# Kernel optimization log

Measured on AMD Instinct MI355X. Metric: run time of the kernel, lower is better.

Reference implementation:

```python
import jax, jax.numpy as jnp
import numpy as np

DIM = 768
NUM_HEADS = 12
HEAD_DIM = 64  # attn_head_dim override
ALL_HEAD_DIM = NUM_HEADS * HEAD_DIM  # 768
SCALE = HEAD_DIM ** -0.5


def setup_inputs() -> dict:
    key = jax.random.key(0)
    ks = jax.random.split(key, 6)
    B, N = 8, 1024
    x = jax.random.normal(ks[0], (B, N, DIM), dtype=jnp.float32)
    w_qkv = jax.random.normal(ks[1], (3 * ALL_HEAD_DIM, DIM), dtype=jnp.float32) * (DIM ** -0.5)
    q_bias = jnp.zeros((ALL_HEAD_DIM,), dtype=jnp.float32)
    v_bias = jnp.zeros((ALL_HEAD_DIM,), dtype=jnp.float32)
    w_proj = jax.random.normal(ks[2], (DIM, ALL_HEAD_DIM), dtype=jnp.float32) * (ALL_HEAD_DIM ** -0.5)
    b_proj = jnp.zeros((DIM,), dtype=jnp.float32)
    return {"x": x, "w_qkv": w_qkv, "q_bias": q_bias, "v_bias": v_bias,
            "w_proj": w_proj, "b_proj": b_proj}


def reference(x, w_qkv, q_bias, v_bias, w_proj, b_proj):
    B, N, C = x.shape
    # qkv bias: [q_bias, zeros (k has no bias), v_bias]
    qkv_bias = jnp.concatenate([q_bias, jnp.zeros_like(v_bias), v_bias])
    qkv = x @ w_qkv.T + qkv_bias                      # [B, N, 3*ALL_HEAD_DIM]
    qkv = qkv.reshape(B, N, 3, NUM_HEADS, HEAD_DIM).transpose(2, 0, 3, 1, 4)
    q, k, v = qkv[0], qkv[1], qkv[2]                  # each [B, H, N, D]
    attn = jnp.einsum('bhqd,bhkd->bhqk', q * SCALE, k)
    attn = jax.nn.softmax(attn, axis=-1)
    out = jnp.einsum('bhqk,bhkd->bhqd', attn, v)      # [B, H, N, D]
    out = out.transpose(0, 2, 1, 3).reshape(B, N, ALL_HEAD_DIM)
    out = out @ w_proj.T + b_proj                     # [B, N, C]
    return out
```

## Files before the change

kernel.cpp:

```cpp
#include <hip/hip_runtime.h>
#include <hip/hip_bf16.h>

typedef unsigned short u16;
typedef unsigned int u32;
typedef __attribute__((ext_vector_type(4))) float f32x4;
typedef __attribute__((ext_vector_type(16))) float f32x16;
typedef __attribute__((ext_vector_type(8))) short bf16x8;

__device__ inline u16 f2bf(float f) {
    union { float f; u32 u; } v; v.f = f;
    u32 r = v.u + 0x7fff + ((v.u >> 16) & 1);
    return (u16)(r >> 16);
}

__device__ inline f32x4 mfma16(bf16x8 a, bf16x8 b, f32x4 c) {
    return __builtin_amdgcn_mfma_f32_16x16x32_bf16(a, b, c, 0, 0, 0);
}
__device__ inline f32x16 mfma32(bf16x8 a, bf16x8 b, f32x16 c) {
    return __builtin_amdgcn_mfma_f32_32x32x16_bf16(a, b, c, 0, 0, 0);
}
__device__ inline u32 cvtpk(float lo, float hi) {
    u32 r;
    asm("v_cvt_pk_bf16_f32 %0, %1, %2" : "=v"(r) : "v"(lo), "v"(hi));
    return r;
}
__device__ inline float exp2v(float x) {
    float r;
    asm("v_exp_f32 %0, %1" : "=v"(r) : "v"(x));
    return r;
}

__device__ inline void gload_lds16(const void* g, const void* l) {
    __builtin_amdgcn_global_load_lds(
        (const __attribute__((address_space(1))) void*)g,
        (__attribute__((address_space(3))) void*)l, 16, 0, 0);
}

#define QSCALE 0.18033688f

__global__ void cvt_all(const float* __restrict__ x,
                        const float* __restrict__ wq,
                        const float* __restrict__ wp,
                        u16* __restrict__ xb, u16* __restrict__ wqb,
                        u16* __restrict__ wpb) {
    int i = blockIdx.x * 256 + threadIdx.x;
    const float* src; u16* dst; int off;
    if (i < 786432)       { src = x;  dst = xb;  off = i; }
    else if (i < 1007616) { src = wq; dst = wqb; off = i - 786432; }
    else                  { src = wp; dst = wpb; off = i - 1007616; }
    const float4* p = (const float4*)src;
    float4 a = p[2 * off], b = p[2 * off + 1];
    bf16x8 v;
    v[0] = (short)f2bf(a.x); v[1] = (short)f2bf(a.y);
    v[2] = (short)f2bf(a.z); v[3] = (short)f2bf(a.w);
    v[4] = (short)f2bf(b.x); v[5] = (short)f2bf(b.y);
    v[6] = (short)f2bf(b.z); v[7] = (short)f2bf(b.w);
    ((bf16x8*)dst)[off] = v;
}

template <int EPI>
__global__ __launch_bounds__(256) void gemm_bt2(
    const u16* __restrict__ A, const u16* __restrict__ B,
    int nbn,
    u16* __restrict__ qw, u16* __restrict__ kw, u16* __restrict__ vw,
    const float* __restrict__ qb, const float* __restrict__ vb,
    float* __restrict__ outp, const float* __restrict__ bproj)
{
    __shared__ __align__(16) u16 smem[16384];
    const int K = 768;
    const int NT = 24;
    const int tid = threadIdx.x;
    const int lane = tid & 63, wv = tid >> 6;
    const int nwg = gridDim.x;
    const int wg = (blockIdx.x & 7) * (nwg >> 3) + (blockIdx.x >> 3);
    const int bm = wg / nbn, bn = wg % nbn;
    const int row0 = bm << 7, col0 = bn << 7;

    const int srow = tid >> 2;
    const int sch = (tid & 3) ^ ((srow >> 1) & 3);
    const u16* gA = A + (size_t)(row0 + srow) * K + sch * 8;
    const u16* gB = B + (size_t)(col0 + srow) * K + sch * 8;
    const int ldst = wv * 512;

    auto stageTile = [&](int bufi, int t) {
        u16* base = &smem[bufi * 8192];
        const int k0 = t << 5;
        gload_lds16(gA + k0,                   base + ldst);
        gload_lds16(gA + (size_t)64 * K + k0,  base + 2048 + ldst);
        gload_lds16(gB + k0,                   base + 4096 + ldst);
        gload_lds16(gB + (size_t)64 * K + k0,  base + 4096 + 2048 + ldst);
    };

    const int wr = (wv >> 1) << 6;
    const int wc = (wv & 1) << 6;
    const int arl = lane & 15, ahi = lane >> 4;
    bf16x8 fa[4], fb[4];
    auto loadFrags = [&](int bufi) {
        const u16* bA = &smem[bufi * 8192];
        const u16* bB = &smem[bufi * 8192 + 4096];
#pragma unroll
        for (int fi = 0; fi < 4; ++fi) {
            const int rl = wr + fi * 16 + arl;
            fa[fi] = *(const bf16x8*)(bA + rl * 32 + ((ahi ^ ((rl >> 1) & 3)) << 3));
        }
#pragma unroll
        for (int fj = 0; fj < 4; ++fj) {
            const int cl = wc + fj * 16 + arl;
            fb[fj] = *(const bf16x8*)(bB + cl * 32 + ((ahi ^ ((cl >> 1) & 3)) << 3));
        }
    };

    f32x4 acc[4][4];
#pragma unroll
    for (int i = 0; i < 4; i++)
#pragma unroll
        for (int j = 0; j < 4; j++) acc[i][j] = (f32x4){0.f, 0.f, 0.f, 0.f};

    auto mfmaTile = [&]() {
        __builtin_amdgcn_s_setprio(1);
#pragma unroll
        for (int i = 0; i < 4; i++)
#pragma unroll
            for (int j = 0; j < 4; j++)
                acc[i][j] = mfma16(fa[i], fb[j], acc[i][j]);
        __builtin_amdgcn_s_setprio(0);
    };

    stageTile(0, 0); stageTile(1, 1);

#pragma unroll 1
    for (int t = 0; t < NT - 1; ++t) {
        asm volatile("s_waitcnt vmcnt(4)" ::: "memory");
        __builtin_amdgcn_s_barrier();
        loadFrags(t & 1);
        asm volatile("s_waitcnt lgkmcnt(0)" ::: "memory");
        __builtin_amdgcn_sched_barrier(0);
        __builtin_amdgcn_s_barrier();
        if (t < NT - 2) stageTile(t & 1, t + 2);
        __builtin_amdgcn_sched_barrier(0);
        mfmaTile();
    }
    asm volatile("s_waitcnt vmcnt(0)" ::: "memory");
    __builtin_amdgcn_s_barrier();
    loadFrags((NT - 1) & 1);
    asm volatile("s_waitcnt lgkmcnt(0)" ::: "memory");
    __builtin_amdgcn_sched_barrier(0);
    mfmaTile();
    __syncthreads();

    if (EPI == 0) {
        const int part = col0 / 768;
        const int colr0 = col0 - part * 768;
        const int h0 = colr0 >> 6;
        const int bb = row0 >> 10;
        const int n0 = row0 & 1023;

        if (part < 2) {
#pragma unroll
            for (int nj = 0; nj < 4; ++nj) {
                const int col = wc + nj * 16 + arl;
                const float bias = (part == 0) ? qb[colr0 + col] : 0.f;
                const float sc = (part == 0) ? QSCALE : 1.f;
#pragma unroll
                for (int mi = 0; mi < 4; ++mi) {
#pragma unroll
                    for (int j = 0; j < 4; ++j) {
                        const int row = wr + mi * 16 + (ahi << 2) + j;
                        smem[row * 128 + ((((col >> 3) ^ (row & 7)) << 3) | (col & 7))] =
                            f2bf((acc[mi][nj][j] + bias) * sc);
                    }
                }
            }
        } else {
#pragma unroll
            for (int nj = 0; nj < 4; ++nj) {
                const int col = wc + nj * 16 + arl;
                const float bias = vb[colr0 + col];
#pragma unroll
                for (int mi = 0; mi < 4; ++mi) {
                    const int row = wr + mi * 16 + (ahi << 2);
                    ushort4 pk;
                    pk.x = f2bf(acc[mi][nj][0] + bias);
                    pk.y = f2bf(acc[mi][nj][1] + bias);
                    pk.z = f2bf(acc[mi][nj][2] + bias);
                    pk.w = f2bf(acc[mi][nj][3] + bias);
                    *(ushort4*)&smem[col * 128 +
                        ((((row >> 3) ^ (col & 7)) << 3) | (row & 7))] = pk;
                }
            }
        }
        __syncthreads();

        if (part == 0) {
#pragma unroll
            for (int p = 0; p < 8; ++p) {
                const int c = p * 256 + tid;
                const int h = c >> 10, ri = (c >> 3) & 127, j = c & 7;
                bf16x8 v = *(const bf16x8*)&smem[ri * 128 + ((((h << 3) + j) ^ (ri & 7)) << 3)];
                *(bf16x8*)&qw[((size_t)(((bb * 12 + h0 + h) << 10) + n0 + ri)) * 64 + j * 8] = v;
            }
        } else if (part == 1) {
#pragma unroll
            for (int p = 0; p < 8; ++p) {
                const int c = p * 256 + tid;
                const int h = c >> 10, t2 = (c >> 8) & 3, j = (c >> 5) & 7, r = c & 31;
                const int ri = t2 * 32 + r;
                bf16x8 v = *(const bf16x8*)&smem[ri * 128 + ((((h << 3) + j) ^ (ri & 7)) << 3)];
                *(bf16x8*)&kw[((size_t)(bb * 12 + h0 + h) << 16) +
                              (((n0 >> 5) + t2) << 11) + (j << 8) + (r << 3)] = v;
            }
        } else {
#pragma unroll
            for (int p = 0; p < 8; ++p) {
                const int c = p * 256 + tid;
                const int h = c >> 10, w = c & 1023;
                const int t2 = w >> 8, f = (w >> 6) & 3, ln = w & 63;
                const int d = ((f >> 1) << 5) + (ln & 31);
                const int rb_ = t2 * 32 + ((f & 1) << 4) + ((ln >> 5) << 3);
                const int ct = h * 64 + d;
                bf16x8 v = *(const bf16x8*)&smem[ct * 128 + (((rb_ >> 3) ^ (ct & 7)) << 3)];
                *(bf16x8*)&vw[((size_t)(bb * 12 + h0 + h) << 16) +
                              (((n0 >> 5) + t2) << 11) + (f << 9) + (ln << 3)] = v;
            }
        }
    } else {
        const int N = nbn << 7;
#pragma unroll
        for (int nj = 0; nj < 4; ++nj) {
            const int col = col0 + wc + nj * 16 + arl;
            const float bias = bproj[col];
#pragma unroll
            for (int mi = 0; mi < 4; ++mi) {
#pragma unroll
                for (int j = 0; j < 4; ++j) {
                    const int row = row0 + wr + mi * 16 + (ahi << 2) + j;
                    outp[(size_t)row * N + col] = acc[mi][nj][j] + bias;
                }
            }
        }
    }
}

__global__ __launch_bounds__(256, 3) void attn_fwd(
    const u16* __restrict__ Q, const u16* __restrict__ KF,
    const u16* __restrict__ VF, u16* __restrict__ O)
{
    __shared__ __align__(16) u16 tlds[4][32 * 68];
    const int tid = threadIdx.x, lane = tid & 63, wv = tid >> 6;
    const int l31 = lane & 31, hi = lane >> 5;
    const int bh = blockIdx.x % 96;
    const int qbk = blockIdx.x / 96;
    const int q0 = qbk * 128 + wv * 32;
    const size_t base = (size_t)bh << 16;
    const u16* Qp = Q + base;
    const u16* Kp = KF + base;
    const u16* Vp = VF + base;

    bf16x8 qf0, qf1, qf2, qf3;
    {
        const u16* qrow = &Qp[(q0 + l31) * 64 + hi * 8];
        qf0 = *(const bf16x8*)(qrow);
        qf1 = *(const bf16x8*)(qrow + 16);
        qf2 = *(const bf16x8*)(qrow + 32);
        qf3 = *(const bf16x8*)(qrow + 48);
    }

    f32x16 ot0, ot1;
#pragma unroll
    for (int i = 0; i < 16; ++i) { ot0[i] = 0.f; ot1[i] = 0.f; }
    float m = -1e30f, l = 0.f;

    auto loadK = [&](int t2048, bf16x8& f0, bf16x8& f1, bf16x8& f2, bf16x8& f3) {
        const u16* kr = &Kp[t2048 + hi * 256 + l31 * 8];
        f0 = *(const bf16x8*)(kr);
        f1 = *(const bf16x8*)(kr + 512);
        f2 = *(const bf16x8*)(kr + 1024);
        f3 = *(const bf16x8*)(kr + 1536);
    };

    auto body = [&](int t2048, bf16x8 k0, bf16x8 k1, bf16x8 k2, bf16x8 k3) {
        f32x16 s;
#pragma unroll
        for (int i = 0; i < 16; ++i) s[i] = 0.f;
        __builtin_amdgcn_s_setprio(1);
        s = mfma32(k0, qf0, s);
        s = mfma32(k1, qf1, s);
        s = mfma32(k2, qf2, s);
        s = mfma32(k3, qf3, s);
        __builtin_amdgcn_s_setprio(0);
        const u16* vrow = &Vp[t2048 + lane * 8];
        bf16x8 vf00 = *(const bf16x8*)(vrow);
        bf16x8 vf01 = *(const bf16x8*)(vrow + 512);
        bf16x8 vf10 = *(const bf16x8*)(vrow + 1024);
        bf16x8 vf11 = *(const bf16x8*)(vrow + 1536);
        float t0 = fmaxf(fmaxf(s[0], s[1]), fmaxf(s[2], s[3]));
        float t1 = fmaxf(fmaxf(s[4], s[5]), fmaxf(s[6], s[7]));
        float t2 = fmaxf(fmaxf(s[8], s[9]), fmaxf(s[10], s[11]));
        float t3 = fmaxf(fmaxf(s[12], s[13]), fmaxf(s[14], s[15]));
        float tmax = fmaxf(fmaxf(t0, t1), fmaxf(t2, t3));
        tmax = fmaxf(tmax, __shfl_xor(tmax, 32));
        if (!__all(tmax - m <= 8.f)) {
            const float nm = fmaxf(m, tmax);
            const float cr = exp2v(m - nm);
#pragma unroll
            for (int i = 0; i < 16; ++i) { ot0[i] *= cr; ot1[i] *= cr; }
            l *= cr; m = nm;
        }
#pragma unroll
        for (int i = 0; i < 16; ++i) { float p = exp2v(s[i] - m); s[i] = p; l += p; }
        u32 w0 = cvtpk(s[0],  s[1]),  w1 = cvtpk(s[2],  s[3]);
        u32 w2 = cvtpk(s[4],  s[5]),  w3 = cvtpk(s[6],  s[7]);
        u32 w4 = cvtpk(s[8],  s[9]),  w5 = cvtpk(s[10], s[11]);
        u32 w6 = cvtpk(s[12], s[13]), w7 = cvtpk(s[14], s[15]);
        asm("v_permlane32_swap_b32 %0, %1" : "+v"(w0), "+v"(w2));
        asm("v_permlane32_swap_b32 %0, %1" : "+v"(w1), "+v"(w3));
        asm("v_permlane32_swap_b32 %0, %1" : "+v"(w4), "+v"(w6));
        asm("v_permlane32_swap_b32 %0, %1" : "+v"(w5), "+v"(w7));
        union { u32 u[4]; bf16x8 v; } pb0, pb1;
        pb0.u[0] = w0; pb0.u[1] = w1; pb0.u[2] = w2; pb0.u[3] = w3;
        pb1.u[0] = w4; pb1.u[1] = w5; pb1.u[2] = w6; pb1.u[3] = w7;
        __builtin_amdgcn_s_setprio(1);
        ot0 = mfma32(vf00, pb0.v, ot0);
        ot0 = mfma32(vf01, pb1.v, ot0);
        ot1 = mfma32(vf10, pb0.v, ot1);
        ot1 = mfma32(vf11, pb1.v, ot1);
        __builtin_amdgcn_s_setprio(0);
    };

    bf16x8 ka0, ka1, ka2, ka3, kb0, kb1, kb2, kb3;
    loadK(0, ka0, ka1, ka2, ka3);
    for (int kt = 0; kt < 32; kt += 2) {
        loadK((kt + 1) << 11, kb0, kb1, kb2, kb3);
        body(kt << 11, ka0, ka1, ka2, ka3);
        if (kt + 2 < 32) loadK((kt + 2) << 11, ka0, ka1, ka2, ka3);
        body((kt + 1) << 11, kb0, kb1, kb2, kb3);
    }

    const float lt = l + __shfl_xor(l, 32);
    const float inv = 1.f / lt;
    u16* tw = &tlds[wv][0];
    u32* tw32 = (u32*)tw;
#pragma unroll
    for (int i = 0; i < 8; ++i) {
        const int dl = 2 * (i & 1) + 8 * (i >> 1) + 4 * hi;
        tw32[(l31 * 68 + dl) >> 1]      = cvtpk(ot0[2 * i] * inv, ot0[2 * i + 1] * inv);
        tw32[(l31 * 68 + dl + 32) >> 1] = cvtpk(ot1[2 * i] * inv, ot1[2 * i + 1] * inv);
    }
    __syncthreads();
    const int b = bh / 12, h = bh - b * 12;
    const size_t obase = ((size_t)(b << 10) + q0) * 768 + h * 64 + (lane & 7) * 8;
#pragma unroll
    for (int it = 0; it < 4; ++it) {
        const int r = it * 8 + (lane >> 3);
        bf16x8 v = *(const bf16x8*)&tw[r * 68 + (lane & 7) * 8];
        *(bf16x8*)&O[obase + (size_t)r * 768] = v;
    }
}

extern "C" void kernel_launch(void* const* d_in, const int* in_sizes, int n_in,
                              void* d_out, int out_size, void* d_ws, size_t ws_size,
                              hipStream_t stream) {
    const float* x      = (const float*)d_in[0];
    const float* w_qkv  = (const float*)d_in[1];
    const float* q_bias = (const float*)d_in[2];
    const float* v_bias = (const float*)d_in[3];
    const float* w_proj = (const float*)d_in[4];
    const float* b_proj = (const float*)d_in[5];
    float* out = (float*)d_out;

    char* ws = (char*)d_ws;
    u16* xb     = (u16*)(ws);
    u16* wqkvb  = (u16*)(ws + 12582912);
    u16* wprojb = (u16*)(ws + 16121856);
    u16* qw     = (u16*)(ws + 17301504);
    u16* kw     = (u16*)(ws + 29884416);
    u16* vt     = (u16*)(ws + 42467328);
    u16* ob     = (u16*)(ws + 55050240);

    cvt_all<<<4224, 256, 0, stream>>>(x, w_qkv, w_proj, xb, wqkvb, wprojb);

    gemm_bt2<0><<<(8192 / 128) * (2304 / 128), 256, 0, stream>>>(
        xb, wqkvb, 2304 / 128, qw, kw, vt, q_bias, v_bias, nullptr, nullptr);

    attn_fwd<<<96 * 8, 256, 0, stream>>>(qw, kw, vt, ob);

    gemm_bt2<1><<<(8192 / 128) * (768 / 128), 256, 0, stream>>>(
        ob, wprojb, 768 / 128, nullptr, nullptr, nullptr, nullptr, nullptr, out, b_proj);
}
```

Baseline: 110.2 us.

## Pre-swizzle weights into fragment layout and load B directly from global

The conversion kernel now writes the bf16 weight matrices in a tiled fragment-ready layout (128-col by 32-k tiles). The GEMM then loads B fragments straight from global/L2 into registers instead of staging them through LDS. Only A remains double-buffered in shared memory. This cuts LDS traffic and halves the async loads per stage, but the B loads are now exposed global latency inside the loop rather than prefetched two tiles ahead.

```diff
diff --git a/kernel.cpp b/kernel.cpp
--- a/kernel.cpp
+++ b/kernel.cpp
@@ -44,10 +44,10 @@
                         u16* __restrict__ xb, u16* __restrict__ wqb,
                         u16* __restrict__ wpb) {
     int i = blockIdx.x * 256 + threadIdx.x;
-    const float* src; u16* dst; int off;
-    if (i < 786432)       { src = x;  dst = xb;  off = i; }
-    else if (i < 1007616) { src = wq; dst = wqb; off = i - 786432; }
-    else                  { src = wp; dst = wpb; off = i - 1007616; }
+    const float* src; u16* dst; int off; bool frag;
+    if (i < 786432)       { src = x;  dst = xb;  off = i;           frag = false; }
+    else if (i < 1007616) { src = wq; dst = wqb; off = i - 786432;  frag = true;  }
+    else                  { src = wp; dst = wpb; off = i - 1007616; frag = true;  }
     const float4* p = (const float4*)src;
     float4 a = p[2 * off], b = p[2 * off + 1];
     bf16x8 v;
@@ -55,12 +55,18 @@
     v[2] = (short)f2bf(a.z); v[3] = (short)f2bf(a.w);
     v[4] = (short)f2bf(b.x); v[5] = (short)f2bf(b.y);
     v[6] = (short)f2bf(b.z); v[7] = (short)f2bf(b.w);
-    ((bf16x8*)dst)[off] = v;
+    if (!frag) {
+        ((bf16x8*)dst)[off] = v;
+    } else {
+        const int n = off / 96, k8 = off - n * 96;
+        const int addr = (((n >> 7) * 24 + (k8 >> 2)) << 12) + ((n & 127) << 5) + ((k8 & 3) << 3);
+        *(bf16x8*)&dst[addr] = v;
+    }
 }
 
 template <int EPI>
-__global__ __launch_bounds__(256) void gemm_bt2(
-    const u16* __restrict__ A, const u16* __restrict__ B,
+__global__ __launch_bounds__(256) void gemm_bL2(
+    const u16* __restrict__ A, const u16* __restrict__ Bf,
     int nbn,
     u16* __restrict__ qw, u16* __restrict__ kw, u16* __restrict__ vw,
     const float* __restrict__ qb, const float* __restrict__ vb,
@@ -79,35 +85,33 @@
     const int srow = tid >> 2;
     const int sch = (tid & 3) ^ ((srow >> 1) & 3);
     const u16* gA = A + (size_t)(row0 + srow) * K + sch * 8;
-    const u16* gB = B + (size_t)(col0 + srow) * K + sch * 8;
     const int ldst = wv * 512;
 
-    auto stageTile = [&](int bufi, int t) {
-        u16* base = &smem[bufi * 8192];
+    auto stageA = [&](int bufi, int t) {
+        u16* base = &smem[bufi * 4096];
         const int k0 = t << 5;
         gload_lds16(gA + k0,                   base + ldst);
         gload_lds16(gA + (size_t)64 * K + k0,  base + 2048 + ldst);
-        gload_lds16(gB + k0,                   base + 4096 + ldst);
-        gload_lds16(gB + (size_t)64 * K + k0,  base + 4096 + 2048 + ldst);
     };
 
     const int wr = (wv >> 1) << 6;
     const int wc = (wv & 1) << 6;
     const int arl = lane & 15, ahi = lane >> 4;
     bf16x8 fa[4], fb[4];
-    auto loadFrags = [&](int bufi) {
-        const u16* bA = &smem[bufi * 8192];
-        const u16* bB = &smem[bufi * 8192 + 4096];
+    auto loadFragsA = [&](int bufi) {
+        const u16* bA = &smem[bufi * 4096];
 #pragma unroll
         for (int fi = 0; fi < 4; ++fi) {
             const int rl = wr + fi * 16 + arl;
             fa[fi] = *(const bf16x8*)(bA + rl * 32 + ((ahi ^ ((rl >> 1) & 3)) << 3));
         }
-#pragma unroll
-        for (int fj = 0; fj < 4; ++fj) {
-            const int cl = wc + fj * 16 + arl;
-            fb[fj] = *(const bf16x8*)(bB + cl * 32 + ((ahi ^ ((cl >> 1) & 3)) << 3));
-        }
+    };
+    const u16* gBlane = Bf + ((size_t)bn * NT << 12) + ((wc + arl) << 5) + (ahi << 3);
+    auto loadFragsB = [&](int t) {
+        const u16* bt = gBlane + (t << 12);
+#pragma unroll
+        for (int fj = 0; fj < 4; ++fj)
+            fb[fj] = *(const bf16x8*)(bt + fj * 512);
     };
 
     f32x4 acc[4][4];
@@ -126,23 +130,25 @@
         __builtin_amdgcn_s_setprio(0);
     };
 
-    stageTile(0, 0); stageTile(1, 1);
+    stageA(0, 0); stageA(1, 1);
 
 #pragma unroll 1
     for (int t = 0; t < NT - 1; ++t) {
-        asm volatile("s_waitcnt vmcnt(4)" ::: "memory");
+        asm volatile("s_waitcnt vmcnt(2)" ::: "memory");
         __builtin_amdgcn_s_barrier();
-        loadFrags(t & 1);
+        loadFragsB(t);
+        loadFragsA(t & 1);
         asm volatile("s_waitcnt lgkmcnt(0)" ::: "memory");
         __builtin_amdgcn_sched_barrier(0);
         __builtin_amdgcn_s_barrier();
-        if (t < NT - 2) stageTile(t & 1, t + 2);
+        if (t < NT - 2) stageA(t & 1, t + 2);
         __builtin_amdgcn_sched_barrier(0);
         mfmaTile();
     }
     asm volatile("s_waitcnt vmcnt(0)" ::: "memory");
     __builtin_amdgcn_s_barrier();
-    loadFrags((NT - 1) & 1);
+    loadFragsB(NT - 1);
+    loadFragsA((NT - 1) & 1);
     asm volatile("s_waitcnt lgkmcnt(0)" ::: "memory");
     __builtin_amdgcn_sched_barrier(0);
     mfmaTile();
@@ -379,11 +385,11 @@
 
     cvt_all<<<4224, 256, 0, stream>>>(x, w_qkv, w_proj, xb, wqkvb, wprojb);
 
-    gemm_bt2<0><<<(8192 / 128) * (2304 / 128), 256, 0, stream>>>(
+    gemm_bL2<0><<<(8192 / 128) * (2304 / 128), 256, 0, stream>>>(
         xb, wqkvb, 2304 / 128, qw, kw, vt, q_bias, v_bias, nullptr, nullptr);
 
     attn_fwd<<<96 * 8, 256, 0, stream>>>(qw, kw, vt, ob);
 
-    gemm_bt2<1><<<(8192 / 128) * (768 / 128), 256, 0, stream>>>(
+    gemm_bL2<1><<<(8192 / 128) * (768 / 128), 256, 0, stream>>>(
         ob, wprojb, 768 / 128, nullptr, nullptr, nullptr, nullptr, nullptr, out, b_proj);
 }
```

Measured after the change: 131.5 us. 1.19x slower.
